# Optimization experiments

Hardware: AMD Instinct MI355X
Metric: run time of the kernel (lower is better)

The kernel has to match this reference:

```python
import jax, jax.numpy as jnp
import numpy as np

# config matching init_kwargs
C = 256; G = 16; GC = C // G; K = 3; P = K * K
PAD = 1; STR = 1; DIL = 1; OFFSET_SCALE = 1.0
N, H, W = 8, 64, 64


def setup_inputs() -> dict:
    key = jax.random.key(0)
    ks = jax.random.split(key, 8)
    def rn(k, shape, sc):
        return jax.random.normal(k, shape, jnp.float32) * sc
    return {
        "x": jax.random.normal(ks[0], (N, H, W, C), jnp.float32),
        "dw_w": rn(ks[1], (C, 1, K, K), 0.1),          # depthwise conv weight (OIHW, groups=C)
        "dw_b": jnp.zeros((C,), jnp.float32),
        "ln_g": jnp.ones((C,), jnp.float32),
        "ln_b": jnp.zeros((C,), jnp.float32),
        "off_w": rn(ks[2], (G * P * 2, C), 0.01),      # offset head (small so offsets stay sane)
        "off_b": jnp.zeros((G * P * 2,), jnp.float32),
        "mask_w": rn(ks[3], (G * P, C), 0.01),
        "mask_b": jnp.zeros((G * P,), jnp.float32),
        "in_w": rn(ks[4], (C, C), 0.05),
        "in_b": jnp.zeros((C,), jnp.float32),
        "out_w": rn(ks[5], (C, C), 0.05),
        "out_b": jnp.zeros((C,), jnp.float32),
    }


def _layer_norm(x, g, b, eps=1e-6):
    m = x.mean(-1, keepdims=True)
    v = ((x - m) ** 2).mean(-1, keepdims=True)
    return (x - m) * jax.lax.rsqrt(v + eps) * g + b


def _grid_sample_bilinear(img, grid):
    # img: (B, Cc, Hh, Ww); grid: (B, L, P, 2) normalized to [-1, 1], (x, y) order.
    # Matches torch.grid_sample(mode='bilinear', padding_mode='zeros', align_corners=False).
    B, Cc, Hh, Ww = img.shape
    gx = (grid[..., 0] + 1.0) * (Ww * 0.5) - 0.5
    gy = (grid[..., 1] + 1.0) * (Hh * 0.5) - 0.5
    x0 = jnp.floor(gx); y0 = jnp.floor(gy)
    tx = gx - x0; ty = gy - y0
    img_f = img.reshape(B, Cc, Hh * Ww)
    def corner(xi, yi, w):
        valid = (xi >= 0) & (xi < Ww) & (yi >= 0) & (yi < Hh)
        idx = (jnp.clip(yi, 0, Hh - 1) * Ww + jnp.clip(xi, 0, Ww - 1)).astype(jnp.int32)
        v = jnp.take_along_axis(img_f, idx.reshape(B, 1, -1), axis=2)  # (B, Cc, L*P)
        return v * (w * valid).reshape(B, 1, -1)
    out = (corner(x0, y0, (1 - tx) * (1 - ty)) + corner(x0 + 1, y0, tx * (1 - ty))
           + corner(x0, y0 + 1, (1 - tx) * ty) + corner(x0 + 1, y0 + 1, tx * ty))
    return out.reshape(B, Cc, grid.shape[1], grid.shape[2])  # (B, Cc, L, P)


def _dcnv3_core(x, offset, mask):
    # x: (N,H,W,C) value features; offset: (N,H,W,G*P*2); mask: (N,H,W,G*P)
    xpad = jnp.pad(x, ((0, 0), (PAD, PAD), (PAD, PAD), (0, 0)))
    Hi, Wi = H + 2 * PAD, W + 2 * PAD
    Ho, Wo = H, W
    # reference points (centers of receptive field), normalized by padded size
    start = (DIL * (K - 1)) // 2 + 0.5
    ry = (start + jnp.arange(Ho, dtype=jnp.float32) * STR) / Hi
    rx = (start + jnp.arange(Wo, dtype=jnp.float32) * STR) / Wi
    ref = jnp.stack([jnp.broadcast_to(rx[None, :], (Ho, Wo)),
                     jnp.broadcast_to(ry[:, None], (Ho, Wo))], -1)  # (Ho,Wo,2) (x,y)
    # dilation grid, x-major flattening to match torch meshgrid('ij') ordering
    d = jnp.arange(K, dtype=jnp.float32) * DIL - (DIL * (K - 1)) // 2
    kgrid = jnp.stack([jnp.repeat(d, K) / Wi, jnp.tile(d, K) / Hi], -1)  # (P,2)
    off = offset.reshape(N, Ho, Wo, G, P, 2)
    norm = jnp.array([Wi, Hi], jnp.float32)
    loc = (ref[None, :, :, None, None, :]
           + kgrid[None, None, None, None, :, :] * OFFSET_SCALE
           + off * OFFSET_SCALE / norm)                      # (N,Ho,Wo,G,P,2)
    sg = (2.0 * loc - 1.0).reshape(N, Ho * Wo, G, P, 2)
    sg = sg.transpose(0, 2, 1, 3, 4).reshape(N * G, Ho * Wo, P, 2)
    val = xpad.reshape(N, Hi * Wi, G * GC).transpose(0, 2, 1).reshape(N * G, GC, Hi, Wi)
    samp = _grid_sample_bilinear(val, sg)                    # (N*G, GC, Ho*Wo, P)
    m = mask.reshape(N, Ho * Wo, G, P).transpose(0, 2, 1, 3).reshape(N * G, 1, Ho * Wo, P)
    out = (samp * m).sum(-1)                                 # (N*G, GC, Ho*Wo)
    return out.reshape(N, G * GC, Ho * Wo).transpose(0, 2, 1).reshape(N, Ho, Wo, C)


def reference(x, dw_w, dw_b, ln_g, ln_b, off_w, off_b, mask_w, mask_b, in_w, in_b, out_w, out_b):
    xp = x @ in_w.T + in_b                                   # input_proj (values)
    # depthwise conv -> LN (channels_last) -> exact GELU
    y = jax.lax.conv_general_dilated(
        x.transpose(0, 3, 1, 2), dw_w, (1, 1), ((PAD, PAD), (PAD, PAD)),
        feature_group_count=C, dimension_numbers=('NCHW', 'OIHW', 'NCHW'))
    y = y + dw_b[None, :, None, None]
    x1 = jax.nn.gelu(_layer_norm(y.transpose(0, 2, 3, 1), ln_g, ln_b), approximate=False)
    offset = x1 @ off_w.T + off_b                            # (N,H,W,G*P*2)
    mlogits = (x1 @ mask_w.T + mask_b).reshape(N, H, W, G, P)
    mask = jax.nn.softmax(mlogits, axis=-1).reshape(N, H, W, G * P)
    out = _dcnv3_core(xp, offset, mask)
    return out @ out_w.T + out_b
```

## Files before the change

kernel.cpp:

```cpp
#include <hip/hip_runtime.h>


#define LL 32768
#define CC 256

typedef __bf16 bf16;
typedef __bf16 bf16x4 __attribute__((ext_vector_type(4)));
typedef __bf16 bf16x8 __attribute__((ext_vector_type(8)));
typedef float f32x4v __attribute__((ext_vector_type(4)));
typedef float f32x2 __attribute__((ext_vector_type(2)));

__device__ __forceinline__ void gload16(const bf16* g, const bf16* lds_base) {
    __builtin_amdgcn_global_load_lds(
        (const __attribute__((address_space(1))) void*)g,
        (__attribute__((address_space(3))) void*)lds_base, 16, 0, 0);
}

__global__ __launch_bounds__(256) void k_prep(
    const float* __restrict__ in_w, const float* __restrict__ off_w,
    const float* __restrict__ mask_w, const float* __restrict__ out_w,
    const float* __restrict__ dw_w, const float* __restrict__ off_b,
    const float* __restrict__ mask_b,
    bf16* __restrict__ in_h, bf16* __restrict__ hw_h,
    bf16* __restrict__ out_h,
    float* __restrict__ dwT, float* __restrict__ hbias) {
    int idx = blockIdx.x * 256 + threadIdx.x;
    if (idx < 60416) {
        const float* s; bf16* hi; int i;
        if (idx < 16384)      { s = in_w;   hi = in_h;          i = idx; }
        else if (idx < 34816) { s = off_w;  hi = hw_h;          i = idx - 16384; }
        else if (idx < 44032) { s = mask_w; hi = hw_h + 73728;  i = idx - 34816; }
        else                  { s = out_w;  hi = out_h;         i = idx - 44032; }
        float4 v = *(const float4*)(s + (size_t)i * 4);
        bf16x4 h;
        h[0] = (bf16)v.x; h[1] = (bf16)v.y; h[2] = (bf16)v.z; h[3] = (bf16)v.w;
        *(bf16x4*)(hi + (size_t)i * 4) = h;
    } else if (idx < 62720) {
        int e = idx - 60416;
        int c = e & 255, j = e >> 8;
        dwT[j * 256 + c] = dw_w[c * 9 + j];
    } else if (idx < 63232) {
        int e = idx - 62720;
        hbias[e] = (e < 288) ? off_b[e] : (e < 432 ? mask_b[e - 288] : 0.f);
    } else if (idx < 68352) {
        int e = idx - 63232;
        bf16x4 z = {(bf16)0.f, (bf16)0.f, (bf16)0.f, (bf16)0.f};
        *(bf16x4*)(hw_h + 110592 + (size_t)e * 4) = z;
    }
}

__global__ __launch_bounds__(256) void k_dwln(
    const float* __restrict__ x, const float* __restrict__ dwT,
    const float* __restrict__ dw_b, const float* __restrict__ ln_g,
    const float* __restrict__ ln_b, bf16* __restrict__ x1h,
    bf16* __restrict__ xb) {
    int t = threadIdx.x;
    int q = t >> 6, u = t & 63;
    int l = blockIdx.x * 4 + q;
    int w = l & 63, h = (l >> 6) & 63, n = l >> 12;
    int c0 = u * 4;

    float4 acc = *(const float4*)(dw_b + c0);
    float4 xc = {0.f, 0.f, 0.f, 0.f};
#pragma unroll
    for (int kh = 0; kh < 3; ++kh) {
        int hh = h + kh - 1;
        if (hh < 0 || hh >= 64) continue;
#pragma unroll
        for (int kw = 0; kw < 3; ++kw) {
            int ww = w + kw - 1;
            if (ww < 0 || ww >= 64) continue;
            float4 xv = *(const float4*)(x + (size_t)(((n * 64 + hh) * 64) + ww) * CC + c0);
            if (kh == 1 && kw == 1) xc = xv;
            float4 wv = *(const float4*)(dwT + (kh * 3 + kw) * 256 + c0);
            acc.x += xv.x * wv.x; acc.y += xv.y * wv.y;
            acc.z += xv.z * wv.z; acc.w += xv.w * wv.w;
        }
    }
    bf16x4 xcb;
    xcb[0] = (bf16)xc.x; xcb[1] = (bf16)xc.y;
    xcb[2] = (bf16)xc.z; xcb[3] = (bf16)xc.w;
    *(bf16x4*)(xb + (size_t)l * CC + c0) = xcb;

    float s = acc.x + acc.y + acc.z + acc.w;
    float ss = acc.x * acc.x + acc.y * acc.y + acc.z * acc.z + acc.w * acc.w;
#pragma unroll
    for (int d = 1; d < 64; d <<= 1) {
        s += __shfl_xor(s, d);
        ss += __shfl_xor(ss, d);
    }
    float mean = s * (1.0f / 256.0f);
    float var = ss * (1.0f / 256.0f) - mean * mean;
    float rstd = rsqrtf(var + 1e-6f);
    float4 gv = *(const float4*)(ln_g + c0);
    float4 bv = *(const float4*)(ln_b + c0);
    float xn0 = (acc.x - mean) * rstd * gv.x + bv.x;
    float xn1 = (acc.y - mean) * rstd * gv.y + bv.y;
    float xn2 = (acc.z - mean) * rstd * gv.z + bv.z;
    float xn3 = (acc.w - mean) * rstd * gv.w + bv.w;
    bf16x4 oh;
    oh[0] = (bf16)(0.5f * xn0 * (1.0f + erff(xn0 * 0.70710678118654752f)));
    oh[1] = (bf16)(0.5f * xn1 * (1.0f + erff(xn1 * 0.70710678118654752f)));
    oh[2] = (bf16)(0.5f * xn2 * (1.0f + erff(xn2 * 0.70710678118654752f)));
    oh[3] = (bf16)(0.5f * xn3 * (1.0f + erff(xn3 * 0.70710678118654752f)));
    *(bf16x4*)(x1h + (size_t)l * CC + c0) = oh;
}

template <bool OBF16>
__global__ __launch_bounds__(256) void k_gemm(
    const bf16* __restrict__ A, const bf16* __restrict__ Wh,
    const float* __restrict__ bias, float* __restrict__ C32,
    bf16* __restrict__ Cbf, int Nout) {
    int mb = blockIdx.x * 128, nb = blockIdx.y * 128;
    int t = threadIdx.x, wave = t >> 6, lane = t & 63;
    int wm = wave & 1, wn = wave >> 1;
    int fm = lane & 15, fq = lane >> 4;

    __shared__ bf16 smem[8192];

    const bf16* gbase[4];
    const bf16* lbase[4];
#pragma unroll
    for (int j = 0; j < 4; ++j) {
        int seg = wave * 4 + j;
        int arr = seg >> 3;
        int row = (seg & 7) * 16 + (lane >> 2);
        int col = (lane & 3) * 8;
        const bf16* g = (arr == 0) ? (A + (size_t)(mb + row) * CC + col)
                                   : (Wh + (size_t)(nb + row) * CC + col);
        gbase[j] = g;
        lbase[j] = smem + seg * 512;
    }

    f32x4v acc[4][4];
#pragma unroll
    for (int i = 0; i < 4; ++i)
#pragma unroll
        for (int j = 0; j < 4; ++j) acc[i][j] = (f32x4v){0.f, 0.f, 0.f, 0.f};

    for (int kc = 0; kc < 256; kc += 32) {
#pragma unroll
        for (int j = 0; j < 4; ++j) gload16(gbase[j] + kc, lbase[j]);
        __syncthreads();

        bf16x8 af[4], bfh[4];
#pragma unroll
        for (int i = 0; i < 4; ++i)
            af[i] = *(const bf16x8*)&smem[(wm * 64 + i * 16 + fm) * 32 + fq * 8];
#pragma unroll
        for (int j = 0; j < 4; ++j)
            bfh[j] = *(const bf16x8*)&smem[4096 + (wn * 64 + j * 16 + fm) * 32 + fq * 8];
#pragma unroll
        for (int i = 0; i < 4; ++i)
#pragma unroll
            for (int j = 0; j < 4; ++j)
                acc[i][j] = __builtin_amdgcn_mfma_f32_16x16x32_bf16(
                    af[i], bfh[j], acc[i][j], 0, 0, 0);
        __syncthreads();
    }

#pragma unroll
    for (int j = 0; j < 4; ++j) {
        int n_g = nb + wn * 64 + j * 16 + fm;
        if (n_g >= Nout) continue;
        float bv = bias[n_g];
#pragma unroll
        for (int i = 0; i < 4; ++i) {
            int m_g = mb + wm * 64 + i * 16 + fq * 4;
#pragma unroll
            for (int rg = 0; rg < 4; ++rg) {
                float o = acc[i][j][rg] + bv;
                if (OBF16)
                    Cbf[(size_t)(m_g + rg) * Nout + n_g] = (bf16)o;
                else
                    C32[(size_t)(m_g + rg) * Nout + n_g] = o;
            }
        }
    }
}

__device__ __forceinline__ void mac8(f32x2 acc[4], bf16x8 v, float wt) {
    union { bf16x8 b; unsigned u[4]; } cu;
    cu.b = v;
    f32x2 wv = {wt, wt};
#pragma unroll
    for (int i = 0; i < 4; ++i) {
        f32x2 a;
        a.x = __uint_as_float(cu.u[i] << 16);
        a.y = __uint_as_float(cu.u[i] & 0xffff0000u);
        acc[i] += a * wv;
    }
}

__global__ __launch_bounds__(256) void k_gather(
    const bf16* __restrict__ xp, const bf16* __restrict__ head,
    bf16* __restrict__ rows) {
    int t = threadIdx.x;
    int q = t >> 5, u = t & 31;
    int l = blockIdx.x * 8 + q;
    int w = l & 63, h = (l >> 6) & 63, n = l >> 12;

    __shared__ float CW[8][576];
    __shared__ int BASE[8][144];

    for (int j = u; j < 432; j += 32) CW[q][j] = (float)head[(size_t)l * 432 + j];
    __syncthreads();

    if (u < 16) {
        int g = u;
        float mx = -1e30f;
#pragma unroll
        for (int p = 0; p < 9; ++p) mx = fmaxf(mx, CW[q][288 + g * 9 + p]);
        float s = 0.f, e[9];
#pragma unroll
        for (int p = 0; p < 9; ++p) { e[p] = expf(CW[q][288 + g * 9 + p] - mx); s += e[p]; }
        float inv = 1.0f / s;
#pragma unroll
        for (int p = 0; p < 9; ++p) CW[q][288 + g * 9 + p] = e[p] * inv;
    }
    __syncthreads();

    float4 cwr[5];
    int baser[5];
#pragma unroll
    for (int k = 0; k < 5; ++k) {
        if (k < 4 || u < 16) {
            int ei = u + 32 * k;
            int g = ei / 9, p = ei - g * 9;
            float ox = CW[q][g * 18 + p * 2 + 0];
            float oy = CW[q][g * 18 + p * 2 + 1];
            float m  = CW[q][288 + ei];
            float ax = (float)(w + (p / 3) - 1) + ox;
            float ay = (float)(h + (p % 3) - 1) + oy;
            float x0f = floorf(ax), y0f = floorf(ay);
            int x0 = (int)x0f, y0 = (int)y0f;
            float tx = ax - x0f, ty = ay - y0f;
            int xb, yb;
            float wxa, wxb, wya, wyb;
            if (x0 < 0)       { xb = 0;  wxa = (x0 == -1) ? tx : 0.f; wxb = 0.f; }
            else if (x0 > 62) { xb = 62; wxa = 0.f; wxb = (x0 == 63) ? (1.f - tx) : 0.f; }
            else              { xb = x0; wxa = 1.f - tx; wxb = tx; }
            if (y0 < 0)       { yb = 0;  wya = (y0 == -1) ? ty : 0.f; wyb = 0.f; }
            else if (y0 > 62) { yb = 62; wya = 0.f; wyb = (y0 == 63) ? (1.f - ty) : 0.f; }
            else              { yb = y0; wya = 1.f - ty; wyb = ty; }
            float4 cw;
            cw.x = m * wxa * wya; cw.y = m * wxb * wya;
            cw.z = m * wxa * wyb; cw.w = m * wxb * wyb;
            cwr[k] = cw;
            baser[k] = (n << 20) + (yb * 64 + xb) * 256;
        }
    }
    __syncthreads();
#pragma unroll
    for (int k = 0; k < 5; ++k) {
        if (k < 4 || u < 16) {
            int ei = u + 32 * k;
            *(float4*)&CW[q][ei * 4] = cwr[k];
            BASE[q][ei] = baser[k];
        }
    }
    __syncthreads();

    int g = u >> 1;
    int c0 = g * 16 + (u & 1) * 8;
    const bf16* xpc = xp + c0;
    f32x2 acc[4];
    acc[0] = (f32x2){0.f, 0.f}; acc[1] = (f32x2){0.f, 0.f};
    acc[2] = (f32x2){0.f, 0.f}; acc[3] = (f32x2){0.f, 0.f};
#pragma unroll
    for (int p = 0; p < 9; ++p) {
        int ei = g * 9 + p;
        float4 cw = *(const float4*)&CW[q][ei * 4];
        int base = BASE[q][ei];
        const bf16* p0 = xpc + base;
        const bf16* p1 = p0 + 16384;
        bf16x8 v00 = *(const bf16x8*)(p0);
        bf16x8 v01 = *(const bf16x8*)(p0 + 256);
        bf16x8 v10 = *(const bf16x8*)(p1);
        bf16x8 v11 = *(const bf16x8*)(p1 + 256);
        mac8(acc, v00, cw.x);
        mac8(acc, v01, cw.y);
        mac8(acc, v10, cw.z);
        mac8(acc, v11, cw.w);
    }
    bf16x8 oh;
    oh[0] = (bf16)acc[0].x; oh[1] = (bf16)acc[0].y;
    oh[2] = (bf16)acc[1].x; oh[3] = (bf16)acc[1].y;
    oh[4] = (bf16)acc[2].x; oh[5] = (bf16)acc[2].y;
    oh[6] = (bf16)acc[3].x; oh[7] = (bf16)acc[3].y;
    *(bf16x8*)(rows + (size_t)l * CC + c0) = oh;
}

__device__ __forceinline__ float dot256f(const float* a, const float* wrow) {
    const float4* w4 = (const float4*)wrow;
    float s = 0.f;
#pragma unroll 16
    for (int i = 0; i < 64; ++i) {
        float4 u = w4[i];
        const float* ap = a + i * 4;
        s += ap[0] * u.x + ap[1] * u.y + ap[2] * u.z + ap[3] * u.w;
    }
    return s;
}

__global__ __launch_bounds__(256) void k_inproj_fb(
    const float* __restrict__ x, const float* __restrict__ in_w,
    const float* __restrict__ in_b, float* __restrict__ xp) {
    int l = blockIdx.x;
    int t = threadIdx.x;
    __shared__ float xa[256];
    xa[t] = x[l * CC + t];
    __syncthreads();
    xp[l * CC + t] = dot256f(xa, in_w + t * CC) + in_b[t];
}

__device__ __forceinline__ float fetch_px_fb(const float* base, int yy, int xx) {
    if (xx < 0 || xx >= 64 || yy < 0 || yy >= 64) return 0.f;
    return base[(yy * 64 + xx) * CC];
}

__global__ __launch_bounds__(256) void k_main_fb(
    const float* __restrict__ x, const float* __restrict__ xp,
    const float* __restrict__ dw_w, const float* __restrict__ dw_b,
    const float* __restrict__ ln_g, const float* __restrict__ ln_b,
    const float* __restrict__ off_w, const float* __restrict__ off_b,
    const float* __restrict__ mask_w, const float* __restrict__ mask_b,
    const float* __restrict__ out_w, const float* __restrict__ out_b,
    float* __restrict__ out) {
    int l = blockIdx.x;
    int t = threadIdx.x;
    int w = l & 63, h = (l >> 6) & 63, n = l >> 12;
    __shared__ float x1[256];
    __shared__ float red[256];
    __shared__ float offs[288];
    __shared__ float ms[144];
    __shared__ float row[256];

    float acc = dw_b[t];
#pragma unroll
    for (int kh = 0; kh < 3; ++kh) {
        int hh = h + kh - 1;
        if (hh < 0 || hh >= 64) continue;
#pragma unroll
        for (int kw = 0; kw < 3; ++kw) {
            int ww = w + kw - 1;
            if (ww < 0 || ww >= 64) continue;
            acc += x[(((n * 64 + hh) * 64) + ww) * CC + t] * dw_w[t * 9 + kh * 3 + kw];
        }
    }
    red[t] = acc;
    __syncthreads();
    for (int s = 128; s > 0; s >>= 1) {
        if (t < s) red[t] += red[t + s];
        __syncthreads();
    }
    float mean = red[0] * (1.0f / 256.0f);
    __syncthreads();
    float d = acc - mean;
    red[t] = d * d;
    __syncthreads();
    for (int s = 128; s > 0; s >>= 1) {
        if (t < s) red[t] += red[t + s];
        __syncthreads();
    }
    float var = red[0] * (1.0f / 256.0f);
    float xn = d * rsqrtf(var + 1e-6f) * ln_g[t] + ln_b[t];
    x1[t] = 0.5f * xn * (1.0f + erff(xn * 0.70710678118654752f));
    __syncthreads();

    offs[t] = dot256f(x1, off_w + t * CC) + off_b[t];
    if (t < 32) {
        int j = 256 + t;
        offs[j] = dot256f(x1, off_w + j * CC) + off_b[j];
    }
    if (t < 144) ms[t] = dot256f(x1, mask_w + t * CC) + mask_b[t];
    __syncthreads();

    if (t < 16) {
        int g = t;
        float mx = -1e30f;
#pragma unroll
        for (int p = 0; p < 9; ++p) mx = fmaxf(mx, ms[g * 9 + p]);
        float s = 0.f, e[9];
#pragma unroll
        for (int p = 0; p < 9; ++p) { e[p] = expf(ms[g * 9 + p] - mx); s += e[p]; }
        float inv = 1.0f / s;
#pragma unroll
        for (int p = 0; p < 9; ++p) ms[g * 9 + p] = e[p] * inv;
    }
    __syncthreads();

    int g = t >> 4;
    const float* base = xp + (size_t)n * 64 * 64 * CC + t;
    float acc2 = 0.f;
#pragma unroll
    for (int p = 0; p < 9; ++p) {
        float ox = offs[g * 18 + p * 2 + 0];
        float oy = offs[g * 18 + p * 2 + 1];
        float ax = (float)(w + (p / 3) - 1) + ox;
        float ay = (float)(h + (p % 3) - 1) + oy;
        float x0f = floorf(ax), y0f = floorf(ay);
        int x0 = (int)x0f, y0 = (int)y0f;
        float tx = ax - x0f, ty = ay - y0f;
        float v00 = fetch_px_fb(base, y0, x0);
        float v01 = fetch_px_fb(base, y0, x0 + 1);
        float v10 = fetch_px_fb(base, y0 + 1, x0);
        float v11 = fetch_px_fb(base, y0 + 1, x0 + 1);
        float bl = (v00 * (1.f - tx) + v01 * tx) * (1.f - ty) +
                   (v10 * (1.f - tx) + v11 * tx) * ty;
        acc2 += ms[g * 9 + p] * bl;
    }
    row[t] = acc2;
    __syncthreads();
    out[l * CC + t] = dot256f(row, out_w + t * CC) + out_b[t];
}

extern "C" void kernel_launch(void* const* d_in, const int* in_sizes, int n_in,
                              void* d_out, int out_size, void* d_ws,
                              size_t ws_size, hipStream_t stream) {
    const float* x      = (const float*)d_in[0];
    const float* dw_w   = (const float*)d_in[1];
    const float* dw_b   = (const float*)d_in[2];
    const float* ln_g   = (const float*)d_in[3];
    const float* ln_b   = (const float*)d_in[4];
    const float* off_w  = (const float*)d_in[5];
    const float* off_b  = (const float*)d_in[6];
    const float* mask_w = (const float*)d_in[7];
    const float* mask_b = (const float*)d_in[8];
    const float* in_w   = (const float*)d_in[9];
    const float* in_b   = (const float*)d_in[10];
    const float* out_w  = (const float*)d_in[11];
    const float* out_b  = (const float*)d_in[12];
    float* out = (float*)d_out;

    const size_t szBF    = (size_t)LL * CC * 2;
    const size_t szHEADB = (size_t)LL * 432 * 2;
    const size_t szWB    = 1048576;
    const size_t need    = 3 * szBF + szHEADB + szWB;

    dim3 blk(256);
    if (ws_size >= need) {
        char* p = (char*)d_ws;
        bf16* x1h = (bf16*)p; p += szBF;
        bf16* xpb = (bf16*)p; p += szBF;
        bf16* xb  = (bf16*)p; p += szBF;
        bf16* headb = (bf16*)p; p += szHEADB;
        bf16* in_h  = (bf16*)p; p += 131072;
        bf16* hw_h  = (bf16*)p; p += 262144;
        bf16* out_h = (bf16*)p; p += 131072;
        float* dwT  = (float*)p; p += 9216;
        float* hbias = (float*)p;
        bf16* rows = x1h;

        k_prep<<<dim3(267), blk, 0, stream>>>(in_w, off_w, mask_w, out_w, dw_w,
                                              off_b, mask_b, in_h, hw_h, out_h,
                                              dwT, hbias);
        k_dwln<<<dim3(LL / 4), blk, 0, stream>>>(x, dwT, dw_b, ln_g, ln_b, x1h, xb);
        k_gemm<true><<<dim3(256, 2), blk, 0, stream>>>(
            xb, in_h, in_b, nullptr, xpb, 256);
        k_gemm<true><<<dim3(256, 4), blk, 0, stream>>>(
            x1h, hw_h, hbias, nullptr, headb, 432);
        k_gather<<<dim3(LL / 8), blk, 0, stream>>>(xpb, headb, rows);
        k_gemm<false><<<dim3(256, 2), blk, 0, stream>>>(
            rows, out_h, out_b, out, nullptr, 256);
    } else {
        float* xp = (float*)d_ws;
        k_inproj_fb<<<dim3(LL), blk, 0, stream>>>(x, in_w, in_b, xp);
        k_main_fb<<<dim3(LL), blk, 0, stream>>>(x, xp, dw_w, dw_b, ln_g, ln_b,
                                                off_w, off_b, mask_w, mask_b,
                                                out_w, out_b, out);
    }
}
```

Before: 204.2 us.

## Double-buffer GEMM LDS tiles and merge input-proj and head GEMMs into one launch

The GEMM core now double-buffers its K tiles in shared memory. It issues the next tile's global-to-LDS loads before computing on the current tile, which removes one barrier per iteration. The input projection and offset/mask head GEMMs are fused into a single launch with a 6-wide grid y-dimension that picks operands per block. LDS use doubles to 32KB per block, which may lower occupancy. The global_load_lds wait semantics depend on the compiler inserting the proper waitcnt before the barrier.

```diff
diff --git a/kernel.cpp b/kernel.cpp
--- a/kernel.cpp
+++ b/kernel.cpp
@@ -107,29 +107,27 @@
 }
 
 template <bool OBF16>
-__global__ __launch_bounds__(256) void k_gemm(
+__device__ __forceinline__ void gemm_core(
     const bf16* __restrict__ A, const bf16* __restrict__ Wh,
     const float* __restrict__ bias, float* __restrict__ C32,
-    bf16* __restrict__ Cbf, int Nout) {
-    int mb = blockIdx.x * 128, nb = blockIdx.y * 128;
+    bf16* __restrict__ Cbf, int Nout, int mb, int nb) {
     int t = threadIdx.x, wave = t >> 6, lane = t & 63;
     int wm = wave & 1, wn = wave >> 1;
     int fm = lane & 15, fq = lane >> 4;
 
-    __shared__ bf16 smem[8192];
+    __shared__ bf16 smem[16384];
 
     const bf16* gbase[4];
-    const bf16* lbase[4];
+    int lofs[4];
 #pragma unroll
     for (int j = 0; j < 4; ++j) {
         int seg = wave * 4 + j;
         int arr = seg >> 3;
         int row = (seg & 7) * 16 + (lane >> 2);
         int col = (lane & 3) * 8;
-        const bf16* g = (arr == 0) ? (A + (size_t)(mb + row) * CC + col)
-                                   : (Wh + (size_t)(nb + row) * CC + col);
-        gbase[j] = g;
-        lbase[j] = smem + seg * 512;
+        gbase[j] = (arr == 0) ? (A + (size_t)(mb + row) * CC + col)
+                              : (Wh + (size_t)(nb + row) * CC + col);
+        lofs[j] = seg * 512;
     }
 
     f32x4v acc[4][4];
@@ -138,25 +136,31 @@
 #pragma unroll
         for (int j = 0; j < 4; ++j) acc[i][j] = (f32x4v){0.f, 0.f, 0.f, 0.f};
 
-    for (int kc = 0; kc < 256; kc += 32) {
-#pragma unroll
-        for (int j = 0; j < 4; ++j) gload16(gbase[j] + kc, lbase[j]);
+#pragma unroll
+    for (int j = 0; j < 4; ++j) gload16(gbase[j], smem + lofs[j]);
+
+    for (int kt = 0; kt < 8; ++kt) {
+        const bf16* buf = smem + (kt & 1) * 8192;
+        bf16* nxt = smem + ((kt & 1) ^ 1) * 8192;
         __syncthreads();
-
+        if (kt < 7) {
+#pragma unroll
+            for (int j = 0; j < 4; ++j)
+                gload16(gbase[j] + (kt + 1) * 32, nxt + lofs[j]);
+        }
         bf16x8 af[4], bfh[4];
 #pragma unroll
         for (int i = 0; i < 4; ++i)
-            af[i] = *(const bf16x8*)&smem[(wm * 64 + i * 16 + fm) * 32 + fq * 8];
+            af[i] = *(const bf16x8*)&buf[(wm * 64 + i * 16 + fm) * 32 + fq * 8];
 #pragma unroll
         for (int j = 0; j < 4; ++j)
-            bfh[j] = *(const bf16x8*)&smem[4096 + (wn * 64 + j * 16 + fm) * 32 + fq * 8];
+            bfh[j] = *(const bf16x8*)&buf[4096 + (wn * 64 + j * 16 + fm) * 32 + fq * 8];
 #pragma unroll
         for (int i = 0; i < 4; ++i)
 #pragma unroll
             for (int j = 0; j < 4; ++j)
                 acc[i][j] = __builtin_amdgcn_mfma_f32_16x16x32_bf16(
                     af[i], bfh[j], acc[i][j], 0, 0, 0);
-        __syncthreads();
     }
 
 #pragma unroll
@@ -177,6 +181,31 @@
             }
         }
     }
+}
+
+template <bool OBF16>
+__global__ __launch_bounds__(256) void k_gemm(
+    const bf16* __restrict__ A, const bf16* __restrict__ Wh,
+    const float* __restrict__ bias, float* __restrict__ C32,
+    bf16* __restrict__ Cbf, int Nout) {
+    gemm_core<OBF16>(A, Wh, bias, C32, Cbf, Nout,
+                     blockIdx.x * 128, blockIdx.y * 128);
+}
+
+__global__ __launch_bounds__(256) void k_gemm_ih(
+    const bf16* __restrict__ xb, const bf16* __restrict__ x1h,
+    const bf16* __restrict__ in_h, const bf16* __restrict__ hw_h,
+    const float* __restrict__ in_b, const float* __restrict__ hbias,
+    bf16* __restrict__ xpb, bf16* __restrict__ headb) {
+    int mb = blockIdx.x * 128;
+    int y = blockIdx.y;
+    const bf16 *A, *W;
+    const float* bs;
+    bf16* Cb;
+    int Nout, nb;
+    if (y < 2) { A = xb;  W = in_h; bs = in_b;  Cb = xpb;   Nout = 256; nb = y * 128; }
+    else       { A = x1h; W = hw_h; bs = hbias; Cb = headb; Nout = 432; nb = (y - 2) * 128; }
+    gemm_core<true>(A, W, bs, nullptr, Cb, Nout, mb, nb);
 }
 
 __device__ __forceinline__ void mac8(f32x2 acc[4], bf16x8 v, float wt) {
@@ -456,10 +485,8 @@
                                               off_b, mask_b, in_h, hw_h, out_h,
                                               dwT, hbias);
         k_dwln<<<dim3(LL / 4), blk, 0, stream>>>(x, dwT, dw_b, ln_g, ln_b, x1h, xb);
-        k_gemm<true><<<dim3(256, 2), blk, 0, stream>>>(
-            xb, in_h, in_b, nullptr, xpb, 256);
-        k_gemm<true><<<dim3(256, 4), blk, 0, stream>>>(
-            x1h, hw_h, hbias, nullptr, headb, 432);
+        k_gemm_ih<<<dim3(256, 6), blk, 0, stream>>>(
+            xb, x1h, in_h, hw_h, in_b, hbias, xpb, headb);
         k_gather<<<dim3(LL / 8), blk, 0, stream>>>(xpb, headb, rows);
         k_gemm<false><<<dim3(256, 2), blk, 0, stream>>>(
             rows, out_h, out_b, out, nullptr, 256);
```

After: 199.1 us. 2.5% less time.
